# Kernel optimization log

Hardware: AMD Instinct MI355X
Metric: run time of the kernel (lower is better)

Reference implementation:

```python
import jax, jax.numpy as jnp
import numpy as np

EMBED_DIM = 1024
NUM_HEADS = 16
HEAD_DIM = EMBED_DIM // NUM_HEADS


def setup_inputs() -> dict:
    key = jax.random.key(0)
    ks = jax.random.split(key, 5)
    s = 1.0 / np.sqrt(EMBED_DIM)
    x = jax.random.normal(ks[0], (2, 2048, EMBED_DIM), dtype=jnp.float32)
    wq = jax.random.normal(ks[1], (EMBED_DIM, EMBED_DIM), dtype=jnp.float32) * s
    wk = jax.random.normal(ks[2], (EMBED_DIM, EMBED_DIM), dtype=jnp.float32) * s
    wv = jax.random.normal(ks[3], (EMBED_DIM, EMBED_DIM), dtype=jnp.float32) * s
    wo = jax.random.normal(ks[4], (EMBED_DIM, EMBED_DIM), dtype=jnp.float32) * s
    z = jnp.zeros((EMBED_DIM,), dtype=jnp.float32)
    return {"x": x, "wq": wq, "bq": z, "wk": wk, "bk": z, "wv": wv, "bv": z, "wo": wo, "bo": z}


def reference(x, wq, bq, wk, bk, wv, bv, wo, bo):
    B, S, D = x.shape
    H, Hd = NUM_HEADS, HEAD_DIM
    # projections -> [B, H, S, Hd]
    def proj(w, b):
        return (x @ w + b).reshape(B, S, H, Hd).transpose(0, 2, 1, 3)
    q = proj(wq, bq)
    k = proj(wk, bk)
    v = proj(wv, bv)
    scores = jnp.einsum('bhsd,bhtd->bhst', q, k) / jnp.sqrt(jnp.float32(Hd))
    probs = jax.nn.softmax(scores, axis=-1)
    attn = jnp.einsum('bhst,bhtd->bhsd', probs, v)  # [B,H,S,Hd]
    attn = attn.transpose(0, 2, 1, 3).reshape(B, S, D)
    return attn @ wo + bo
```

## Files before the change

### kernel.cpp

```cpp
#include <hip/hip_runtime.h>
#include <cstdint>

typedef __bf16 bf16_t;
typedef __bf16 bf16x4 __attribute__((ext_vector_type(4)));
typedef __bf16 bf16x8 __attribute__((ext_vector_type(8)));
typedef float floatx4 __attribute__((ext_vector_type(4)));

#define EMBED 1024
#define NHEAD 16
#define HDIM  64
#define SEQ   2048
#define BATCH 2
#define MTOT  (BATCH*SEQ)
#define QSCALE 0.18033688011112042f

__device__ __forceinline__ void gload16(const bf16_t* g, bf16_t* l) {
    __builtin_amdgcn_global_load_lds(
        (const __attribute__((address_space(1))) void*)g,
        (__attribute__((address_space(3))) void*)l, 16, 0, 0);
}

__global__ __launch_bounds__(256) void transpose4(
    const float* __restrict__ w0, const float* __restrict__ w1,
    const float* __restrict__ w2, const float* __restrict__ w3,
    const float* __restrict__ xin,
    bf16_t* __restrict__ out, bf16_t* __restrict__ xout)
{
    int z = blockIdx.z;
    int tx = threadIdx.x, ty = threadIdx.y;
    if (z >= 4) {
        const float* src = xin  + (size_t)(z - 4) * 1048576u;
        bf16_t*      dst = xout + (size_t)(z - 4) * 1048576u;
        int col = blockIdx.x * 32 + tx, rowb = blockIdx.y * 32;
#pragma unroll
        for (int j = 0; j < 4; j++) {
            int rr = rowb + ty + 8 * j;
            dst[(size_t)rr * 1024 + col] = (bf16_t)src[(size_t)rr * 1024 + col];
        }
        return;
    }
    __shared__ float t[32][33];
    const float* src = (z == 0) ? w0 : (z == 1) ? w1 : (z == 2) ? w2 : w3;
    bf16_t* dst = out + (size_t)z * 1048576u;
    int bx = blockIdx.x * 32, by = blockIdx.y * 32;
#pragma unroll
    for (int j = 0; j < 4; j++)
        t[ty + 8 * j][tx] = src[(size_t)(by + ty + 8 * j) * EMBED + bx + tx];
    __syncthreads();
#pragma unroll
    for (int j = 0; j < 4; j++)
        dst[(size_t)(bx + ty + 8 * j) * EMBED + by + tx] = (bf16_t)t[tx][ty + 8 * j];
}

template<int BM, int MODE>
__global__ __launch_bounds__(256) void gemm_t(
    const bf16_t* __restrict__ A,  const bf16_t* __restrict__ Bt,
    const float* __restrict__ bias0, const float* __restrict__ bias1,
    const float* __restrict__ bias2,
    void* __restrict__ outraw, bf16_t* __restrict__ vtout,
    int M, int N, int K)
{
    constexpr int MS = BM / 32;
    __shared__ __align__(16) bf16_t smem[BM * 64 + 128 * 64];
    bf16_t (*As)[64] = (bf16_t(*)[64])smem;
    bf16_t (*Bs)[64] = (bf16_t(*)[64])(smem + BM * 64);

    int tid  = threadIdx.x;
    int m0   = blockIdx.y * BM, n0 = blockIdx.x * 128;
    int wv   = tid >> 6, lane = tid & 63;
    int wr   = wv >> 1,  wc   = wv & 1;
    int quad = lane >> 4, l16 = lane & 15;
    int lr   = lane >> 3;
    int lcs  = (((lane & 7) ^ lr) * 8);
    int sw   = (l16 & 7) * 8;

    floatx4 acc[MS][4];
    floatx4 z4 = {0.f, 0.f, 0.f, 0.f};
#pragma unroll
    for (int mi = 0; mi < MS; mi++)
#pragma unroll
        for (int ni = 0; ni < 4; ni++) acc[mi][ni] = z4;

    for (int k0 = 0; k0 < K; k0 += 64) {
        __syncthreads();
#pragma unroll
        for (int i = 0; i < BM / 32; i++) {
            int r = wv * (BM / 4) + i * 8 + lr;
            gload16(&A[(size_t)(m0 + r) * K + k0 + lcs], &As[wv * (BM / 4) + i * 8][0]);
        }
#pragma unroll
        for (int i = 0; i < 4; i++) {
            int r = wv * 32 + i * 8 + lr;
            gload16(&Bt[(size_t)(n0 + r) * K + k0 + lcs], &Bs[wv * 32 + i * 8][0]);
        }
        __syncthreads();
#pragma unroll
        for (int kk = 0; kk < 2; kk++) {
            bf16x8 af[MS], bfr[4];
            int co = kk * 32 + quad * 8;
#pragma unroll
            for (int i = 0; i < MS; i++)
                af[i]  = *(const bf16x8*)&As[wr * (BM / 2) + i * 16 + l16][co ^ sw];
#pragma unroll
            for (int i = 0; i < 4; i++)
                bfr[i] = *(const bf16x8*)&Bs[wc * 64 + i * 16 + l16][co ^ sw];
#pragma unroll
            for (int mi = 0; mi < MS; mi++)
#pragma unroll
                for (int ni = 0; ni < 4; ni++)
                    acc[mi][ni] = __builtin_amdgcn_mfma_f32_16x16x32_bf16(
                        af[mi], bfr[ni], acc[mi][ni], 0, 0, 0);
        }
    }

    if constexpr (MODE == 1) {
        if (n0 >= 2048) {
            bf16_t (*Ts)[72] = (bf16_t(*)[72])smem;
            int bb = m0 >> 11, s0 = m0 & 2047;
            int hd0 = n0 & 1023;
#pragma unroll
            for (int mh = 0; mh < 2; mh++) {
                __syncthreads();
                if (wr == mh) {
#pragma unroll
                    for (int mi = 0; mi < MS; mi++)
#pragma unroll
                        for (int ni = 0; ni < 4; ni++)
#pragma unroll
                            for (int r = 0; r < 4; r++) {
                                int ml = mi * 16 + quad * 4 + r;
                                int nl = wc * 64 + ni * 16 + l16;
                                float v = acc[mi][ni][r] + bias2[hd0 + nl];
                                int sp = 4 * (ml & 15) + (ml >> 4);
                                Ts[nl][sp] = (bf16_t)v;
                            }
                }
                __syncthreads();
#pragma unroll
                for (int i = 0; i < 4; i++) {
                    int c = tid + i * 256;
                    int row = c >> 3, ch = (c & 7) * 8;
                    int hh = row >> 6, dd = row & 63;
                    size_t off = (((size_t)bb * NHEAD + (hd0 >> 6) + hh) * HDIM + dd) * SEQ
                               + (size_t)(s0 + mh * 64 + ch);
                    *(bf16x8*)&vtout[off] = *(const bf16x8*)&Ts[row][ch];
                }
            }
            return;
        }
    }

#pragma unroll
    for (int mi = 0; mi < MS; mi++) {
#pragma unroll
        for (int ni = 0; ni < 4; ni++) {
            int n = n0 + wc * 64 + ni * 16 + l16;
#pragma unroll
            for (int r = 0; r < 4; r++) {
                int m = m0 + wr * (BM / 2) + mi * 16 + quad * 4 + r;
                float v = acc[mi][ni][r];
                if (MODE == 0) {
                    ((float*)outraw)[(size_t)m * N + n] = v + bias0[n];
                } else {
                    int which = n >> 10, cc = n & 1023;
                    v += (which == 0) ? bias0[cc] : bias1[cc];
                    if (which == 0) v *= QSCALE;
                    int h = cc >> 6, d = cc & 63;
                    int b = m >> 11, s = m & 2047;
                    ((bf16_t*)outraw)[(size_t)which * 4194304u +
                        (((size_t)b * NHEAD + h) * SEQ + s) * HDIM + d] = (bf16_t)v;
                }
            }
        }
    }
}

__global__ __launch_bounds__(256) void attn_mfma(
    const bf16_t* __restrict__ Q, const bf16_t* __restrict__ K,
    const bf16_t* __restrict__ Vt, bf16_t* __restrict__ O)
{
    __shared__ __align__(16) bf16_t Ks[2][64][64];
    __shared__ __align__(16) bf16_t Vs[2][64][64];
    __shared__ __align__(16) bf16_t Ps[4][16][64];

    int tid  = threadIdx.x;
    int wv   = tid >> 6, lane = tid & 63;
    int quad = lane >> 4, l16 = lane & 15;
    int lr   = lane >> 3;
    int lcs  = (((lane & 7) ^ lr) * 8);
    int sw   = (l16 & 7) * 8;
    int flat = blockIdx.x;
    int hb   = flat & 31;
    int qt   = flat >> 5;
    int h = hb & 15, b = hb >> 4;
    int bh = b * NHEAD + h;
    int qw = qt * 64 + wv * 16;

    const bf16_t* Qb = Q  + (size_t)bh * SEQ * HDIM;
    const bf16_t* Kb = K  + (size_t)bh * SEQ * HDIM;
    const bf16_t* Vb = Vt + (size_t)bh * SEQ * HDIM;

    const bf16_t* kg = Kb + (size_t)(wv * 16 + lr) * HDIM + lcs;
    const bf16_t* vg = Vb + (size_t)(wv * 16 + lr) * SEQ + lcs;

    bf16x8 qf[2];
#pragma unroll
    for (int kk = 0; kk < 2; kk++)
        qf[kk] = *(const bf16x8*)&Qb[(size_t)(qw + l16) * HDIM + kk * 32 + quad * 8];

    floatx4 o_acc[4];
    floatx4 z4  = {0.f, 0.f, 0.f, 0.f};
    floatx4 m16 = {-16.f, -16.f, -16.f, -16.f};
#pragma unroll
    for (int nd = 0; nd < 4; nd++) o_acc[nd] = z4;
    float l_i[4] = {0.f, 0.f, 0.f, 0.f};

    {
        gload16(kg,            &Ks[0][wv * 16][0]);
        gload16(kg + 512,      &Ks[0][wv * 16 + 8][0]);
        gload16(vg,            &Vs[0][wv * 16][0]);
        gload16(vg + 8 * SEQ,  &Vs[0][wv * 16 + 8][0]);
    }

    for (int t = 0; t < 32; t++) {
        int cur = t & 1;
        __syncthreads();
        if (t < 31) {
            const bf16_t* kn = kg + (t + 1) * 4096;
            const bf16_t* vn = vg + (t + 1) * 64;
            int nb = cur ^ 1;
            gload16(kn,           &Ks[nb][wv * 16][0]);
            gload16(kn + 512,     &Ks[nb][wv * 16 + 8][0]);
            gload16(vn,           &Vs[nb][wv * 16][0]);
            gload16(vn + 8 * SEQ, &Vs[nb][wv * 16 + 8][0]);
        }

        floatx4 s_acc[4];
#pragma unroll
        for (int ns = 0; ns < 4; ns++) s_acc[ns] = m16;
#pragma unroll
        for (int ns = 0; ns < 4; ns++) {
#pragma unroll
            for (int kk = 0; kk < 2; kk++) {
                bf16x8 kf = *(const bf16x8*)
                    &Ks[cur][ns * 16 + l16][(kk * 32 + quad * 8) ^ sw];
                s_acc[ns] = __builtin_amdgcn_mfma_f32_16x16x32_bf16(
                    qf[kk], kf, s_acc[ns], 0, 0, 0);
            }
        }

#pragma unroll
        for (int r = 0; r < 4; r++) {
            int row = quad * 4 + r;
            float p0 = __builtin_amdgcn_exp2f(s_acc[0][r]);
            float p1 = __builtin_amdgcn_exp2f(s_acc[1][r]);
            float p2 = __builtin_amdgcn_exp2f(s_acc[2][r]);
            float p3 = __builtin_amdgcn_exp2f(s_acc[3][r]);
            l_i[r] += (p0 + p1) + (p2 + p3);
            bf16x4 pk = { (bf16_t)p0, (bf16_t)p1, (bf16_t)p2, (bf16_t)p3 };
            *(bf16x4*)&Ps[wv][row][((l16 >> 1) ^ (row & 7)) * 8 + (l16 & 1) * 4] = pk;
        }

        bf16x8 pf[2];
#pragma unroll
        for (int kk = 0; kk < 2; kk++)
            pf[kk] = *(const bf16x8*)
                &Ps[wv][l16][((kk * 4 + quad) ^ (l16 & 7)) * 8];
#pragma unroll
        for (int nd = 0; nd < 4; nd++) {
#pragma unroll
            for (int kk = 0; kk < 2; kk++) {
                bf16x8 vf = *(const bf16x8*)
                    &Vs[cur][nd * 16 + l16][(kk * 32 + quad * 8) ^ sw];
                o_acc[nd] = __builtin_amdgcn_mfma_f32_16x16x32_bf16(
                    pf[kk], vf, o_acc[nd], 0, 0, 0);
            }
        }
    }

#pragma unroll
    for (int r = 0; r < 4; r++) {
        float l = l_i[r];
        l += __shfl_xor(l, 1);
        l += __shfl_xor(l, 2);
        l += __shfl_xor(l, 4);
        l += __shfl_xor(l, 8);
        float inv = 1.f / l;
        int s = qw + quad * 4 + r;
#pragma unroll
        for (int nd = 0; nd < 4; nd++)
            O[((size_t)b * SEQ + s) * EMBED + h * HDIM + nd * 16 + l16] =
                (bf16_t)(o_acc[nd][r] * inv);
    }
}

extern "C" void kernel_launch(void* const* d_in, const int* in_sizes, int n_in,
                              void* d_out, int out_size, void* d_ws, size_t ws_size,
                              hipStream_t stream)
{
    const float* x  = (const float*)d_in[0];
    const float* wq = (const float*)d_in[1];
    const float* bq = (const float*)d_in[2];
    const float* wk = (const float*)d_in[3];
    const float* bk = (const float*)d_in[4];
    const float* wv = (const float*)d_in[5];
    const float* bv = (const float*)d_in[6];
    const float* wo = (const float*)d_in[7];
    const float* bo = (const float*)d_in[8];

    char*   ws    = (char*)d_ws;
    bf16_t* Wt    = (bf16_t*)ws;
    bf16_t* Xb    = (bf16_t*)(ws + 8ull  * 1024 * 1024);
    bf16_t* QKV   = (bf16_t*)(ws + 16ull * 1024 * 1024);
    bf16_t* Vt    = (bf16_t*)(ws + 40ull * 1024 * 1024);
    bf16_t* attnO = (bf16_t*)(ws + 48ull * 1024 * 1024);
    float*  outp  = (float*)d_out;

    transpose4<<<dim3(32, 32, 8), dim3(32, 8), 0, stream>>>(
        wq, wk, wv, wo, x, Wt, Xb);

    gemm_t<128, 1><<<dim3(24, 32), 256, 0, stream>>>(
        Xb, Wt, bq, bk, bv, QKV, Vt, MTOT, 3072, EMBED);

    attn_mfma<<<dim3(1024), 256, 0, stream>>>(
        QKV, QKV + 4194304u, Vt, attnO);

    gemm_t<64, 0><<<dim3(8, 64), 256, 0, stream>>>(
        attnO, Wt + 3u * 1048576u, bo, bo, bo, outp, nullptr, MTOT, EMBED, EMBED);
}
```

Baseline: 205.5 us.

## Replace direct global-to-LDS loads with register-staged prefetch pipelines

Both the GEMM and the attention kernel stop using global_load_lds and instead load tiles into registers, then write them to swizzled LDS. The GEMM prefetches the next K tile into registers while the MFMAs run on the current one. The attention loop is unrolled by two with two register stage buffers so global loads overlap compute across the double-buffered LDS. The aim is to hide global latency better, at the cost of more VGPRs and explicit LDS write instructions, which may lower occupancy.

```diff
diff --git a/kernel.cpp b/kernel.cpp
--- a/kernel.cpp
+++ b/kernel.cpp
@@ -13,12 +13,6 @@
 #define BATCH 2
 #define MTOT  (BATCH*SEQ)
 #define QSCALE 0.18033688011112042f
-
-__device__ __forceinline__ void gload16(const bf16_t* g, bf16_t* l) {
-    __builtin_amdgcn_global_load_lds(
-        (const __attribute__((address_space(1))) void*)g,
-        (__attribute__((address_space(3))) void*)l, 16, 0, 0);
-}
 
 __global__ __launch_bounds__(256) void transpose4(
     const float* __restrict__ w0, const float* __restrict__ w1,
@@ -61,6 +55,7 @@
     int M, int N, int K)
 {
     constexpr int MS = BM / 32;
+    constexpr int NA = BM / 32;
     __shared__ __align__(16) bf16_t smem[BM * 64 + 128 * 64];
     bf16_t (*As)[64] = (bf16_t(*)[64])smem;
     bf16_t (*Bs)[64] = (bf16_t(*)[64])(smem + BM * 64);
@@ -70,9 +65,9 @@
     int wv   = tid >> 6, lane = tid & 63;
     int wr   = wv >> 1,  wc   = wv & 1;
     int quad = lane >> 4, l16 = lane & 15;
-    int lr   = lane >> 3;
-    int lcs  = (((lane & 7) ^ lr) * 8);
+    int lr   = lane >> 3, lq = lane & 7;
     int sw   = (l16 & 7) * 8;
+    int wch  = (lq ^ lr) * 8;
 
     floatx4 acc[MS][4];
     floatx4 z4 = {0.f, 0.f, 0.f, 0.f};
@@ -81,19 +76,31 @@
 #pragma unroll
         for (int ni = 0; ni < 4; ni++) acc[mi][ni] = z4;
 
+    bf16x8 sa[NA], sb[4];
+    auto LOADG = [&](int k0) {
+#pragma unroll
+        for (int i = 0; i < NA; i++)
+            sa[i] = *(const bf16x8*)
+                &A[(size_t)(m0 + wv * (BM / 4) + i * 8 + lr) * K + k0 + lq * 8];
+#pragma unroll
+        for (int i = 0; i < 4; i++)
+            sb[i] = *(const bf16x8*)
+                &Bt[(size_t)(n0 + wv * 32 + i * 8 + lr) * K + k0 + lq * 8];
+    };
+    auto STOREG = [&]() {
+#pragma unroll
+        for (int i = 0; i < NA; i++)
+            *(bf16x8*)&As[wv * (BM / 4) + i * 8 + lr][wch] = sa[i];
+#pragma unroll
+        for (int i = 0; i < 4; i++)
+            *(bf16x8*)&Bs[wv * 32 + i * 8 + lr][wch] = sb[i];
+    };
+
+    LOADG(0);
     for (int k0 = 0; k0 < K; k0 += 64) {
+        STOREG();
         __syncthreads();
-#pragma unroll
-        for (int i = 0; i < BM / 32; i++) {
-            int r = wv * (BM / 4) + i * 8 + lr;
-            gload16(&A[(size_t)(m0 + r) * K + k0 + lcs], &As[wv * (BM / 4) + i * 8][0]);
-        }
-#pragma unroll
-        for (int i = 0; i < 4; i++) {
-            int r = wv * 32 + i * 8 + lr;
-            gload16(&Bt[(size_t)(n0 + r) * K + k0 + lcs], &Bs[wv * 32 + i * 8][0]);
-        }
-        __syncthreads();
+        if (k0 + 64 < K) LOADG(k0 + 64);
 #pragma unroll
         for (int kk = 0; kk < 2; kk++) {
             bf16x8 af[MS], bfr[4];
@@ -111,6 +118,7 @@
                     acc[mi][ni] = __builtin_amdgcn_mfma_f32_16x16x32_bf16(
                         af[mi], bfr[ni], acc[mi][ni], 0, 0, 0);
         }
+        if (k0 + 64 < K) __syncthreads();
     }
 
     if constexpr (MODE == 1) {
@@ -186,8 +194,7 @@
     int tid  = threadIdx.x;
     int wv   = tid >> 6, lane = tid & 63;
     int quad = lane >> 4, l16 = lane & 15;
-    int lr   = lane >> 3;
-    int lcs  = (((lane & 7) ^ lr) * 8);
+    int lr   = lane >> 3, lq = lane & 7;
     int sw   = (l16 & 7) * 8;
     int flat = blockIdx.x;
     int hb   = flat & 31;
@@ -200,8 +207,13 @@
     const bf16_t* Kb = K  + (size_t)bh * SEQ * HDIM;
     const bf16_t* Vb = Vt + (size_t)bh * SEQ * HDIM;
 
-    const bf16_t* kg = Kb + (size_t)(wv * 16 + lr) * HDIM + lcs;
-    const bf16_t* vg = Vb + (size_t)(wv * 16 + lr) * SEQ + lcs;
+    int srow = wv * 16 + lr;
+    const bf16_t* kg = Kb + (size_t)srow * HDIM + lq * 8;
+    const bf16_t* vg = Vb + (size_t)srow * SEQ  + lq * 8;
+    bf16_t* kd0 = &Ks[0][srow][(lq ^ lr) * 8];
+    bf16_t* kd1 = &Ks[0][srow + 8][(lq ^ lr) * 8];
+    bf16_t* vd0 = &Vs[0][srow][(lq ^ lr) * 8];
+    bf16_t* vd1 = &Vs[0][srow + 8][(lq ^ lr) * 8];
 
     bf16x8 qf[2];
 #pragma unroll
@@ -215,26 +227,22 @@
     for (int nd = 0; nd < 4; nd++) o_acc[nd] = z4;
     float l_i[4] = {0.f, 0.f, 0.f, 0.f};
 
-    {
-        gload16(kg,            &Ks[0][wv * 16][0]);
-        gload16(kg + 512,      &Ks[0][wv * 16 + 8][0]);
-        gload16(vg,            &Vs[0][wv * 16][0]);
-        gload16(vg + 8 * SEQ,  &Vs[0][wv * 16 + 8][0]);
-    }
-
-    for (int t = 0; t < 32; t++) {
-        int cur = t & 1;
-        __syncthreads();
-        if (t < 31) {
-            const bf16_t* kn = kg + (t + 1) * 4096;
-            const bf16_t* vn = vg + (t + 1) * 64;
-            int nb = cur ^ 1;
-            gload16(kn,           &Ks[nb][wv * 16][0]);
-            gload16(kn + 512,     &Ks[nb][wv * 16 + 8][0]);
-            gload16(vn,           &Vs[nb][wv * 16][0]);
-            gload16(vn + 8 * SEQ, &Vs[nb][wv * 16 + 8][0]);
-        }
-
+    bf16x8 stgA[4], stgB[4];
+    auto LOADT = [&](int t, bf16x8* s) {
+        const bf16_t* kt = kg + (size_t)t * 4096;
+        const bf16_t* vt = vg + (size_t)t * 64;
+        s[0] = *(const bf16x8*)kt;
+        s[1] = *(const bf16x8*)(kt + 8 * HDIM);
+        s[2] = *(const bf16x8*)vt;
+        s[3] = *(const bf16x8*)(vt + 8 * SEQ);
+    };
+    auto STORET = [&](int nb, const bf16x8* s) {
+        *(bf16x8*)(kd0 + nb * 4096) = s[0];
+        *(bf16x8*)(kd1 + nb * 4096) = s[1];
+        *(bf16x8*)(vd0 + nb * 4096) = s[2];
+        *(bf16x8*)(vd1 + nb * 4096) = s[3];
+    };
+    auto COMPUTE = [&](int cur) {
         floatx4 s_acc[4];
 #pragma unroll
         for (int ns = 0; ns < 4; ns++) s_acc[ns] = m16;
@@ -248,7 +256,6 @@
                     qf[kk], kf, s_acc[ns], 0, 0, 0);
             }
         }
-
 #pragma unroll
         for (int r = 0; r < 4; r++) {
             int row = quad * 4 + r;
@@ -260,7 +267,6 @@
             bf16x4 pk = { (bf16_t)p0, (bf16_t)p1, (bf16_t)p2, (bf16_t)p3 };
             *(bf16x4*)&Ps[wv][row][((l16 >> 1) ^ (row & 7)) * 8 + (l16 & 1) * 4] = pk;
         }
-
         bf16x8 pf[2];
 #pragma unroll
         for (int kk = 0; kk < 2; kk++)
@@ -276,6 +282,21 @@
                     pf[kk], vf, o_acc[nd], 0, 0, 0);
             }
         }
+    };
+
+    LOADT(0, stgA);
+    LOADT(1, stgB);
+    STORET(0, stgA);
+
+    for (int tt = 0; tt < 32; tt += 2) {
+        __syncthreads();
+        if (tt + 2 < 32) LOADT(tt + 2, stgA);
+        COMPUTE(0);
+        STORET(1, stgB);
+        __syncthreads();
+        if (tt + 3 < 32) LOADT(tt + 3, stgB);
+        COMPUTE(1);
+        if (tt + 2 < 32) STORET(0, stgA);
     }
 
 #pragma unroll
```

Result: no change. 202.7 us (-1.4%).

## Compute transposed attention tiles in registers and prefetch GEMM tiles through registers

Applied to the files above, without the earlier changes.

The attention kernel now handles 32 query rows per wave, with half as many blocks. It computes S^T by swapping MFMA operands so the exponentiated probabilities land directly in the B-operand register layout, which removes the per-tile shared-memory round trip for P and reuses each K and V fragment across two query subtiles. The GEMM switches from direct global-to-LDS loads to a register-staged software prefetch of the next k-tile, and the V transpose staging permutation is changed to match. The trade-offs are higher register pressure, lower occupancy and fewer blocks in attention.

```diff
diff --git a/kernel.cpp b/kernel.cpp
--- a/kernel.cpp
+++ b/kernel.cpp
@@ -61,6 +61,7 @@
     int M, int N, int K)
 {
     constexpr int MS = BM / 32;
+    constexpr int NA = BM / 32;
     __shared__ __align__(16) bf16_t smem[BM * 64 + 128 * 64];
     bf16_t (*As)[64] = (bf16_t(*)[64])smem;
     bf16_t (*Bs)[64] = (bf16_t(*)[64])(smem + BM * 64);
@@ -70,9 +71,9 @@
     int wv   = tid >> 6, lane = tid & 63;
     int wr   = wv >> 1,  wc   = wv & 1;
     int quad = lane >> 4, l16 = lane & 15;
-    int lr   = lane >> 3;
-    int lcs  = (((lane & 7) ^ lr) * 8);
+    int lr   = lane >> 3, lq = lane & 7;
     int sw   = (l16 & 7) * 8;
+    int wch  = (lq ^ lr) * 8;
 
     floatx4 acc[MS][4];
     floatx4 z4 = {0.f, 0.f, 0.f, 0.f};
@@ -81,19 +82,31 @@
 #pragma unroll
         for (int ni = 0; ni < 4; ni++) acc[mi][ni] = z4;
 
+    bf16x8 sa[NA], sb[4];
+    auto LOADG = [&](int k0) {
+#pragma unroll
+        for (int i = 0; i < NA; i++)
+            sa[i] = *(const bf16x8*)
+                &A[(size_t)(m0 + wv * (BM / 4) + i * 8 + lr) * K + k0 + lq * 8];
+#pragma unroll
+        for (int i = 0; i < 4; i++)
+            sb[i] = *(const bf16x8*)
+                &Bt[(size_t)(n0 + wv * 32 + i * 8 + lr) * K + k0 + lq * 8];
+    };
+    auto STOREG = [&]() {
+#pragma unroll
+        for (int i = 0; i < NA; i++)
+            *(bf16x8*)&As[wv * (BM / 4) + i * 8 + lr][wch] = sa[i];
+#pragma unroll
+        for (int i = 0; i < 4; i++)
+            *(bf16x8*)&Bs[wv * 32 + i * 8 + lr][wch] = sb[i];
+    };
+
+    LOADG(0);
     for (int k0 = 0; k0 < K; k0 += 64) {
+        STOREG();
         __syncthreads();
-#pragma unroll
-        for (int i = 0; i < BM / 32; i++) {
-            int r = wv * (BM / 4) + i * 8 + lr;
-            gload16(&A[(size_t)(m0 + r) * K + k0 + lcs], &As[wv * (BM / 4) + i * 8][0]);
-        }
-#pragma unroll
-        for (int i = 0; i < 4; i++) {
-            int r = wv * 32 + i * 8 + lr;
-            gload16(&Bt[(size_t)(n0 + r) * K + k0 + lcs], &Bs[wv * 32 + i * 8][0]);
-        }
-        __syncthreads();
+        if (k0 + 64 < K) LOADG(k0 + 64);
 #pragma unroll
         for (int kk = 0; kk < 2; kk++) {
             bf16x8 af[MS], bfr[4];
@@ -111,6 +124,7 @@
                     acc[mi][ni] = __builtin_amdgcn_mfma_f32_16x16x32_bf16(
                         af[mi], bfr[ni], acc[mi][ni], 0, 0, 0);
         }
+        if (k0 + 64 < K) __syncthreads();
     }
 
     if constexpr (MODE == 1) {
@@ -131,7 +145,8 @@
                                 int ml = mi * 16 + quad * 4 + r;
                                 int nl = wc * 64 + ni * 16 + l16;
                                 float v = acc[mi][ni][r] + bias2[hd0 + nl];
-                                int sp = 4 * (ml & 15) + (ml >> 4);
+                                int sp = ((ml >> 5) << 5) | (((ml >> 2) & 3) << 3)
+                                       | (((ml >> 4) & 1) << 2) | (ml & 3);
                                 Ts[nl][sp] = (bf16_t)v;
                             }
                 }
@@ -181,53 +196,54 @@
 {
     __shared__ __align__(16) bf16_t Ks[2][64][64];
     __shared__ __align__(16) bf16_t Vs[2][64][64];
-    __shared__ __align__(16) bf16_t Ps[4][16][64];
 
     int tid  = threadIdx.x;
     int wv   = tid >> 6, lane = tid & 63;
     int quad = lane >> 4, l16 = lane & 15;
-    int lr   = lane >> 3;
-    int lcs  = (((lane & 7) ^ lr) * 8);
+    int lr   = lane >> 3, lq = lane & 7;
     int sw   = (l16 & 7) * 8;
     int flat = blockIdx.x;
     int hb   = flat & 31;
     int qt   = flat >> 5;
     int h = hb & 15, b = hb >> 4;
     int bh = b * NHEAD + h;
-    int qw = qt * 64 + wv * 16;
+    int qw = qt * 128 + wv * 32;
 
     const bf16_t* Qb = Q  + (size_t)bh * SEQ * HDIM;
     const bf16_t* Kb = K  + (size_t)bh * SEQ * HDIM;
     const bf16_t* Vb = Vt + (size_t)bh * SEQ * HDIM;
 
-    const bf16_t* kg = Kb + (size_t)(wv * 16 + lr) * HDIM + lcs;
-    const bf16_t* vg = Vb + (size_t)(wv * 16 + lr) * SEQ + lcs;
-
-    bf16x8 qf[2];
-#pragma unroll
-    for (int kk = 0; kk < 2; kk++)
-        qf[kk] = *(const bf16x8*)&Qb[(size_t)(qw + l16) * HDIM + kk * 32 + quad * 8];
-
-    floatx4 o_acc[4];
+    const bf16_t* kg = Kb + (size_t)(wv * 16 + lr) * HDIM + (lq ^ lr) * 8;
+    const bf16_t* vg = Vb + (size_t)(wv * 16 + lr) * SEQ  + (lq ^ lr) * 8;
+
+    bf16x8 qf[2][2];
+#pragma unroll
+    for (int ms = 0; ms < 2; ms++)
+#pragma unroll
+        for (int kk = 0; kk < 2; kk++)
+            qf[ms][kk] = *(const bf16x8*)
+                &Qb[(size_t)(qw + ms * 16 + l16) * HDIM + kk * 32 + quad * 8];
+
+    floatx4 o_acc[2][4];
     floatx4 z4  = {0.f, 0.f, 0.f, 0.f};
     floatx4 m16 = {-16.f, -16.f, -16.f, -16.f};
 #pragma unroll
-    for (int nd = 0; nd < 4; nd++) o_acc[nd] = z4;
-    float l_i[4] = {0.f, 0.f, 0.f, 0.f};
-
-    {
-        gload16(kg,            &Ks[0][wv * 16][0]);
-        gload16(kg + 512,      &Ks[0][wv * 16 + 8][0]);
-        gload16(vg,            &Vs[0][wv * 16][0]);
-        gload16(vg + 8 * SEQ,  &Vs[0][wv * 16 + 8][0]);
-    }
+    for (int ms = 0; ms < 2; ms++)
+#pragma unroll
+        for (int nd = 0; nd < 4; nd++) o_acc[ms][nd] = z4;
+    float l_i[2] = {0.f, 0.f};
+
+    gload16(kg,           &Ks[0][wv * 16][0]);
+    gload16(kg + 512,     &Ks[0][wv * 16 + 8][0]);
+    gload16(vg,           &Vs[0][wv * 16][0]);
+    gload16(vg + 8 * SEQ, &Vs[0][wv * 16 + 8][0]);
 
     for (int t = 0; t < 32; t++) {
         int cur = t & 1;
         __syncthreads();
         if (t < 31) {
-            const bf16_t* kn = kg + (t + 1) * 4096;
-            const bf16_t* vn = vg + (t + 1) * 64;
+            const bf16_t* kn = kg + (size_t)(t + 1) * 4096;
+            const bf16_t* vn = vg + (size_t)(t + 1) * 64;
             int nb = cur ^ 1;
             gload16(kn,           &Ks[nb][wv * 16][0]);
             gload16(kn + 512,     &Ks[nb][wv * 16 + 8][0]);
@@ -235,62 +251,66 @@
             gload16(vn + 8 * SEQ, &Vs[nb][wv * 16 + 8][0]);
         }
 
-        floatx4 s_acc[4];
-#pragma unroll
-        for (int ns = 0; ns < 4; ns++) s_acc[ns] = m16;
+        floatx4 st[2][4];
+#pragma unroll
+        for (int ms = 0; ms < 2; ms++)
+#pragma unroll
+            for (int ns = 0; ns < 4; ns++) st[ms][ns] = m16;
 #pragma unroll
         for (int ns = 0; ns < 4; ns++) {
 #pragma unroll
             for (int kk = 0; kk < 2; kk++) {
                 bf16x8 kf = *(const bf16x8*)
                     &Ks[cur][ns * 16 + l16][(kk * 32 + quad * 8) ^ sw];
-                s_acc[ns] = __builtin_amdgcn_mfma_f32_16x16x32_bf16(
-                    qf[kk], kf, s_acc[ns], 0, 0, 0);
+#pragma unroll
+                for (int ms = 0; ms < 2; ms++)
+                    st[ms][ns] = __builtin_amdgcn_mfma_f32_16x16x32_bf16(
+                        kf, qf[ms][kk], st[ms][ns], 0, 0, 0);
             }
         }
 
-#pragma unroll
-        for (int r = 0; r < 4; r++) {
-            int row = quad * 4 + r;
-            float p0 = __builtin_amdgcn_exp2f(s_acc[0][r]);
-            float p1 = __builtin_amdgcn_exp2f(s_acc[1][r]);
-            float p2 = __builtin_amdgcn_exp2f(s_acc[2][r]);
-            float p3 = __builtin_amdgcn_exp2f(s_acc[3][r]);
-            l_i[r] += (p0 + p1) + (p2 + p3);
-            bf16x4 pk = { (bf16_t)p0, (bf16_t)p1, (bf16_t)p2, (bf16_t)p3 };
-            *(bf16x4*)&Ps[wv][row][((l16 >> 1) ^ (row & 7)) * 8 + (l16 & 1) * 4] = pk;
-        }
-
-        bf16x8 pf[2];
-#pragma unroll
-        for (int kk = 0; kk < 2; kk++)
-            pf[kk] = *(const bf16x8*)
-                &Ps[wv][l16][((kk * 4 + quad) ^ (l16 & 7)) * 8];
+        bf16x8 pf[2][2];
+#pragma unroll
+        for (int ms = 0; ms < 2; ms++) {
+            float ls = 0.f;
+#pragma unroll
+            for (int kk = 0; kk < 2; kk++)
+#pragma unroll
+                for (int tt = 0; tt < 8; tt++) {
+                    float p = __builtin_amdgcn_exp2f(st[ms][2 * kk + (tt >> 2)][tt & 3]);
+                    ls += p;
+                    pf[ms][kk][tt] = (bf16_t)p;
+                }
+            l_i[ms] += ls;
+        }
+
 #pragma unroll
         for (int nd = 0; nd < 4; nd++) {
 #pragma unroll
             for (int kk = 0; kk < 2; kk++) {
                 bf16x8 vf = *(const bf16x8*)
                     &Vs[cur][nd * 16 + l16][(kk * 32 + quad * 8) ^ sw];
-                o_acc[nd] = __builtin_amdgcn_mfma_f32_16x16x32_bf16(
-                    pf[kk], vf, o_acc[nd], 0, 0, 0);
+#pragma unroll
+                for (int ms = 0; ms < 2; ms++)
+                    o_acc[ms][nd] = __builtin_amdgcn_mfma_f32_16x16x32_bf16(
+                        vf, pf[ms][kk], o_acc[ms][nd], 0, 0, 0);
             }
         }
     }
 
 #pragma unroll
-    for (int r = 0; r < 4; r++) {
-        float l = l_i[r];
-        l += __shfl_xor(l, 1);
-        l += __shfl_xor(l, 2);
-        l += __shfl_xor(l, 4);
-        l += __shfl_xor(l, 8);
+    for (int ms = 0; ms < 2; ms++) {
+        float l = l_i[ms];
+        l += __shfl_xor(l, 16);
+        l += __shfl_xor(l, 32);
         float inv = 1.f / l;
-        int s = qw + quad * 4 + r;
+        int q = qw + ms * 16 + l16;
+        bf16_t* ob = O + ((size_t)b * SEQ + q) * EMBED + h * HDIM;
 #pragma unroll
         for (int nd = 0; nd < 4; nd++)
-            O[((size_t)b * SEQ + s) * EMBED + h * HDIM + nd * 16 + l16] =
-                (bf16_t)(o_acc[nd][r] * inv);
+#pragma unroll
+            for (int r = 0; r < 4; r++)
+                ob[nd * 16 + quad * 4 + r] = (bf16_t)(o_acc[ms][nd][r] * inv);
     }
 }
 
@@ -322,7 +342,7 @@
     gemm_t<128, 1><<<dim3(24, 32), 256, 0, stream>>>(
         Xb, Wt, bq, bk, bv, QKV, Vt, MTOT, 3072, EMBED);
 
-    attn_mfma<<<dim3(1024), 256, 0, stream>>>(
+    attn_mfma<<<dim3(512), 256, 0, stream>>>(
         QKV, QKV + 4194304u, Vt, attnO);
 
     gemm_t<64, 0><<<dim3(8, 64), 256, 0, stream>>>(
```

Result: faster. 193.3 us (-6.0%).
